# Optimization experiments

Hardware: AMD Instinct MI355X
Metric: run time of the kernel (lower is better)

The kernel has to match this reference:

```python
import jax, jax.numpy as jnp
import numpy as np

B, P, IN_DIM, OUT_DIM = 4, 120000, 4, 64
SPATIAL = (480, 360, 32)
EPS = 1e-5
SLOPE = 0.01  # LeakyReLU default negative slope


def setup_inputs() -> dict:
    key = jax.random.key(0)
    ks = jax.random.split(key, 10)
    pc = jax.random.normal(ks[0], (B, P, IN_DIM), dtype=jnp.float32)
    pc_indices = jax.random.randint(ks[1], (B, P, 3), 0, 32, dtype=jnp.int32)
    W1 = jax.random.normal(ks[2], (IN_DIM, 16), dtype=jnp.float32) * (1.0 / np.sqrt(IN_DIM))
    b1 = jax.random.normal(ks[3], (16,), dtype=jnp.float32) * 0.01
    g1 = jnp.ones((16,), jnp.float32)
    be1 = jnp.zeros((16,), jnp.float32)
    W2 = jax.random.normal(ks[4], (16, OUT_DIM), dtype=jnp.float32) * 0.25
    b2 = jax.random.normal(ks[5], (OUT_DIM,), dtype=jnp.float32) * 0.01
    g2 = jnp.ones((OUT_DIM,), jnp.float32)
    be2 = jnp.zeros((OUT_DIM,), jnp.float32)
    return {"pc": pc, "pc_indices": pc_indices, "W1": W1, "b1": b1, "g1": g1,
            "be1": be1, "W2": W2, "b2": b2, "g2": g2, "be2": be2}


def _bn_lrelu(h, g, b):
    # BatchNorm1d in training mode: batch mean / biased variance over points
    mean = jnp.mean(h, axis=0)
    var = jnp.mean((h - mean) ** 2, axis=0)
    h = (h - mean) / jnp.sqrt(var + EPS) * g + b
    return jnp.where(h >= 0, h, SLOPE * h)


def reference(pc, pc_indices, W1, b1, g1, be1, W2, b2, g2, be2):
    N = B * P
    x = pc.reshape(N, IN_DIM)
    bid = jnp.repeat(jnp.arange(B, dtype=jnp.int32), P)  # batch id padded in front
    coords = jnp.concatenate([bid[:, None], pc_indices.reshape(N, 3)], axis=1)  # [N,4]

    # small MLP (shuffle/recover in the original is a mathematical no-op for outputs)
    h = _bn_lrelu(x @ W1 + b1, g1, be1)
    feat = _bn_lrelu(h @ W2 + b2, g2, be2)  # [N, OUT_DIM]

    # torch.unique(dim=0) == lexicographic sort of linearized voxel keys
    S0, S1, S2 = SPATIAL
    key = (((coords[:, 0] * S0 + coords[:, 1]) * S1 + coords[:, 2]) * S2 + coords[:, 3])
    order = jnp.argsort(key)
    sk = key[order]
    is_first = jnp.concatenate([jnp.ones((1,), bool), sk[1:] != sk[:-1]])
    seg_sorted = (jnp.cumsum(is_first) - 1).astype(jnp.int32)  # segment id per sorted point
    inv = jnp.zeros((N,), jnp.int32).at[order].set(seg_sorted)  # inverse index (unsorted)

    # scatter_max into (padded, fixed-shape) voxel feature table
    voxel_feat = jax.ops.segment_max(feat, inv, num_segments=N)  # [N, OUT_DIM]
    n_uni = seg_sorted[-1] + 1
    valid = jnp.arange(N) < n_uni
    voxel_feat = jnp.where(valid[:, None], voxel_feat, 0.0)
    voxel_ind = jnp.zeros((N, 4), jnp.int32).at[seg_sorted].set(coords[order])

    return voxel_feat, voxel_ind, feat
```

## Files before the change

kernel.cpp:

```cpp
#include <hip/hip_runtime.h>

typedef unsigned int u32;
typedef unsigned long long u64;

#define N_PTS 480000
#define PPB   120000
#define NKEY  131072
#define NBLK_A 256
#define NBLK_B 512
#define NT64   7500
#define SLOPE 0.01f

__global__ __launch_bounds__(256) void kZ(u32* __restrict__ cnt) {
    uint4 z; z.x = 0u; z.y = 0u; z.z = 0u; z.w = 0u;
    ((uint4*)cnt)[blockIdx.x * 256 + threadIdx.x] = z;
}

__global__ __launch_bounds__(256) void kA(const float* __restrict__ pc,
                                          const int* __restrict__ pidx,
                                          u32* __restrict__ keys,
                                          u32* __restrict__ cnt,
                                          float* __restrict__ pA) {
    int t = threadIdx.x;
    float a[14];
#pragma unroll
    for (int j = 0; j < 14; ++j) a[j] = 0.f;

    for (int n = blockIdx.x * 256 + t; n < N_PTS; n += gridDim.x * 256) {
        float4 x = ((const float4*)pc)[n];
        a[0] += x.x; a[1] += x.y; a[2] += x.z; a[3] += x.w;
        a[4] += x.x * x.x; a[5] += x.x * x.y; a[6]  += x.x * x.z; a[7]  += x.x * x.w;
        a[8] += x.y * x.y; a[9] += x.y * x.z; a[10] += x.y * x.w;
        a[11] += x.z * x.z; a[12] += x.z * x.w; a[13] += x.w * x.w;

        int i0 = pidx[3 * n], i1 = pidx[3 * n + 1], i2 = pidx[3 * n + 2];
        int bid = n / PPB;
        u32 key = (u32)(bid * 32768 + i0 * 1024 + i1 * 32 + i2);
        keys[n] = key;
        atomicAdd(&cnt[key], 1u);
    }

    __shared__ float red[256];
    for (int j = 0; j < 14; ++j) {
        red[t] = a[j];
        __syncthreads();
        for (int s = 128; s > 0; s >>= 1) {
            if (t < s) red[t] += red[t + s];
            __syncthreads();
        }
        if (t == 0) pA[j * NBLK_A + blockIdx.x] = red[0];
        __syncthreads();
    }
}

__global__ __launch_bounds__(1024) void kR1(const float* __restrict__ pA,
                                            const float* __restrict__ W1,
                                            const float* __restrict__ b1,
                                            const float* __restrict__ g1,
                                            const float* __restrict__ be1,
                                            float* __restrict__ stats1) {
    int t = threadIdx.x, w = t >> 6, lane = t & 63;
    __shared__ float S[14];
    if (w < 14) {
        const float* p = pA + w * NBLK_A;
        float s = p[lane] + p[lane + 64] + p[lane + 128] + p[lane + 192];
        for (int d = 32; d > 0; d >>= 1) s += __shfl_xor(s, d);
        if (lane == 0) S[w] = s;
    }
    __syncthreads();
    if (t < 16) {
        int c = t;
        double w4[4];
#pragma unroll
        for (int i = 0; i < 4; ++i) w4[i] = W1[i * 16 + c];
        double sx[4] = { S[0], S[1], S[2], S[3] };
        auto sxx = [&](int i, int j) -> double {
            if (i > j) { int k = i; i = j; j = k; }
            int base = (i == 0) ? 4 : (i == 1) ? 8 : (i == 2) ? 11 : 13;
            return (double)S[base + (j - i)];
        };
        double su = 0.0;
        for (int i = 0; i < 4; ++i) su += sx[i] * w4[i];
        double q = 0.0;
        for (int i = 0; i < 4; ++i)
            for (int j = 0; j < 4; ++j) q += w4[i] * w4[j] * sxx(i, j);
        double b = (double)b1[c];
        double sum   = su + b * (double)N_PTS;
        double sumsq = q + 2.0 * b * su + (double)N_PTS * b * b;
        double mean = sum / (double)N_PTS;
        double var  = sumsq / (double)N_PTS - mean * mean;
        float inv = rsqrtf((float)(var + 1e-5));
        float sc = g1[c] * inv;
        stats1[c]      = sc;
        stats1[16 + c] = be1[c] - (float)mean * sc;
    }
}

__global__ __launch_bounds__(256) void kB(const float* __restrict__ pc,
                                          const float* __restrict__ W1,
                                          const float* __restrict__ b1,
                                          const float* __restrict__ stats1,
                                          float* __restrict__ pB) {
    int t = threadIdx.x;
    __shared__ float shx[256];
    __shared__ float shh[64][16];

    int c1 = t & 15;
    float w1c[4];
#pragma unroll
    for (int i = 0; i < 4; ++i) w1c[i] = W1[i * 16 + c1];
    float b1c = b1[c1], sc1 = stats1[c1], sf1 = stats1[16 + c1];

    int pi = 0, pj = 0;
    if (t >= 16 && t < 152) {
        int rem = t - 16, i = 0;
        while (rem >= 16 - i) { rem -= 16 - i; ++i; }
        pi = i; pj = i + rem;
    }

    float acc = 0.f;
    for (int tile = blockIdx.x; tile < NT64; tile += gridDim.x) {
        int base = tile * 64;
        shx[t] = pc[base * 4 + t];
        __syncthreads();
#pragma unroll
        for (int i = 0; i < 4; ++i) {
            int p = (t >> 4) + 16 * i;
            float hp = b1c + shx[p * 4 + 0] * w1c[0] + shx[p * 4 + 1] * w1c[1]
                           + shx[p * 4 + 2] * w1c[2] + shx[p * 4 + 3] * w1c[3];
            float z = hp * sc1 + sf1;
            shh[p][c1] = (z >= 0.f) ? z : SLOPE * z;
        }
        __syncthreads();
        if (t < 16) {
#pragma unroll 4
            for (int p = 0; p < 64; ++p) acc += shh[p][t];
        } else if (t < 152) {
#pragma unroll 4
            for (int p = 0; p < 64; ++p) acc += shh[p][pi] * shh[p][pj];
        }
        __syncthreads();
    }
    if (t < 152) pB[t * NBLK_B + blockIdx.x] = acc;
}

__global__ __launch_bounds__(1024) void kR2(const float* __restrict__ pB,
                                            const float* __restrict__ W2,
                                            const float* __restrict__ b2,
                                            const float* __restrict__ g2,
                                            const float* __restrict__ be2,
                                            float* __restrict__ stats2) {
    int t = threadIdx.x, w = t >> 6, lane = t & 63;
    __shared__ float S[152];
    for (int q = w; q < 152; q += 16) {
        const float* p = pB + q * NBLK_B;
        float s = 0.f;
#pragma unroll
        for (int b = 0; b < 8; ++b) s += p[b * 64 + lane];
        for (int d = 32; d > 0; d >>= 1) s += __shfl_xor(s, d);
        if (lane == 0) S[q] = s;
    }
    __syncthreads();
    if (t < 64) {
        double wv[16];
#pragma unroll
        for (int k = 0; k < 16; ++k) wv[k] = W2[k * 64 + t];
        double sh = 0.0;
        for (int k = 0; k < 16; ++k) sh += wv[k] * (double)S[k];
        auto qidx = [&](int i, int j) { return 16 + i * 16 - (i * (i - 1)) / 2 + (j - i); };
        double q = 0.0;
        for (int i = 0; i < 16; ++i) {
            q += wv[i] * wv[i] * (double)S[qidx(i, i)];
            double t2 = 0.0;
            for (int j = i + 1; j < 16; ++j) t2 += wv[j] * (double)S[qidx(i, j)];
            q += 2.0 * wv[i] * t2;
        }
        double b = (double)b2[t];
        double sum   = sh + b * (double)N_PTS;
        double sumsq = q + 2.0 * b * sh + (double)N_PTS * b * b;
        double mean = sum / (double)N_PTS;
        double var  = sumsq / (double)N_PTS - mean * mean;
        float inv = rsqrtf((float)(var + 1e-5));
        float sc = g2[t] * inv;
        stats2[t]      = sc;
        stats2[64 + t] = be2[t] - (float)mean * sc;
    }
}

__global__ __launch_bounds__(256) void kS1(const u32* __restrict__ cnt,
                                           u32* __restrict__ bsum) {
    int t = threadIdx.x, b = blockIdx.x;
    uint4 c4 = ((const uint4*)cnt)[b * 256 + t];
    u32 cs = c4.x + c4.y + c4.z + c4.w;
    u32 os = (c4.x > 0) + (c4.y > 0) + (c4.z > 0) + (c4.w > 0);
    __shared__ u32 rc[256], ro[256];
    rc[t] = cs; ro[t] = os;
    __syncthreads();
    for (int s = 128; s > 0; s >>= 1) {
        if (t < s) { rc[t] += rc[t + s]; ro[t] += ro[t + s]; }
        __syncthreads();
    }
    if (t == 0) { bsum[2 * b] = rc[0]; bsum[2 * b + 1] = ro[0]; }
}

__global__ __launch_bounds__(256) void kS2(u32* __restrict__ cnt,
                                           const u32* __restrict__ bsum,
                                           u32* __restrict__ startc,
                                           float* __restrict__ vi,
                                           u32* __restrict__ nuni) {
    int t = threadIdx.x, b = blockIdx.x;
    __shared__ u32 sbc[128], sbo[128];
    __shared__ u32 cOff, oOff;
    __shared__ u64 scan[256];
    if (t < 128) { sbc[t] = bsum[2 * t]; sbo[t] = bsum[2 * t + 1]; }

    uint4 c4 = ((const uint4*)cnt)[b * 256 + t];
    u32 cv[4] = { c4.x, c4.y, c4.z, c4.w };
    u32 cs = cv[0] + cv[1] + cv[2] + cv[3];
    u32 os = (cv[0] > 0) + (cv[1] > 0) + (cv[2] > 0) + (cv[3] > 0);
    scan[t] = ((u64)cs << 32) | (u64)os;
    __syncthreads();
    if (t == 0) {
        u32 a = 0, o = 0;
        for (int i = 0; i < b; ++i) { a += sbc[i]; o += sbo[i]; }
        cOff = a; oOff = o;
    }
    for (int d = 1; d < 256; d <<= 1) {
        u64 v = (t >= d) ? scan[t - d] : 0ull;
        __syncthreads();
        scan[t] += v;
        __syncthreads();
    }
    u64 ex = scan[t] - (((u64)cs << 32) | (u64)os);
    u32 start = cOff + (u32)(ex >> 32);
    u32 rank  = oOff + (u32)(ex & 0xffffffffull);

    int kbase = b * 1024 + t * 4;
#pragma unroll
    for (int j = 0; j < 4; ++j) {
        u32 k = (u32)(kbase + j);
        cnt[k] = start;
        if (cv[j] > 0) {
            startc[rank] = start;
            float4 o;
            o.x = (float)(k >> 15);
            o.y = (float)((k >> 10) & 31);
            o.z = (float)((k >> 5) & 31);
            o.w = (float)(k & 31);
            ((float4*)vi)[rank] = o;
            rank++;
        }
        start += cv[j];
    }
    if (b == 127 && t == 255) {
        nuni[0] = rank;
        startc[rank] = N_PTS;
    }
}

__global__ __launch_bounds__(256) void kP(const u32* __restrict__ keys,
                                          u32* __restrict__ cursor,
                                          u32* __restrict__ pid) {
    int n = blockIdx.x * 256 + threadIdx.x;
    if (n < N_PTS) {
        u32 k = keys[n];
        u32 pos = atomicAdd(&cursor[k], 1u);
        pid[pos] = (u32)n;
    }
}

__global__ __launch_bounds__(256) void kC(const float* __restrict__ pc,
                                          const float* __restrict__ W1,
                                          const float* __restrict__ b1,
                                          const float* __restrict__ stats1,
                                          const float* __restrict__ W2,
                                          const float* __restrict__ b2,
                                          const float* __restrict__ stats2,
                                          float* __restrict__ feat_out) {
    int t = threadIdx.x;
    __shared__ float shx[256];
    __shared__ float shh[64][16];

    int c1 = t & 15;
    float w1c[4];
#pragma unroll
    for (int i = 0; i < 4; ++i) w1c[i] = W1[i * 16 + c1];
    float b1c = b1[c1], sc1 = stats1[c1], sf1 = stats1[16 + c1];

    int c2 = t & 63;
    float w2c[16];
#pragma unroll
    for (int k = 0; k < 16; ++k) w2c[k] = W2[k * 64 + c2];
    float b2c = b2[c2], sc2 = stats2[c2], sf2 = stats2[64 + c2];
    int pg = t >> 6;

    for (int tile = blockIdx.x; tile < NT64; tile += gridDim.x) {
        int base = tile * 64;
        shx[t] = pc[base * 4 + t];
        __syncthreads();
#pragma unroll
        for (int i = 0; i < 4; ++i) {
            int p = (t >> 4) + 16 * i;
            float hp = b1c + shx[p * 4 + 0] * w1c[0] + shx[p * 4 + 1] * w1c[1]
                           + shx[p * 4 + 2] * w1c[2] + shx[p * 4 + 3] * w1c[3];
            float z = hp * sc1 + sf1;
            shh[p][c1] = (z >= 0.f) ? z : SLOPE * z;
        }
        __syncthreads();
#pragma unroll
        for (int j = 0; j < 16; ++j) {
            int p = pg + 4 * j;
            float f = b2c;
#pragma unroll
            for (int k = 0; k < 16; ++k) f += shh[p][k] * w2c[k];
            float z = f * sc2 + sf2;
            float ff = (z >= 0.f) ? z : SLOPE * z;
            feat_out[(size_t)(base + p) * 64 + c2] = ff;
        }
        __syncthreads();
    }
}

__global__ __launch_bounds__(256) void kV(const float* __restrict__ feat,
                                          const u32* __restrict__ pid,
                                          const u32* __restrict__ startc,
                                          const u32* __restrict__ nuni,
                                          float* __restrict__ vf,
                                          float* __restrict__ vi) {
    u32 nu = *nuni;
    u32 r0 = blockIdx.x * 4;
    int w = threadIdx.x >> 6, lane = threadIdx.x & 63;

    if (threadIdx.x < 16) {
        u32 row = r0 + (threadIdx.x >> 2);
        if (row >= nu) vi[(size_t)row * 4 + (threadIdx.x & 3)] = 0.f;
    }

    u32 r = r0 + (u32)w;
    if (r < nu) {
        u32 s = startc[r], e = startc[r + 1];
        float m = -3.4e38f;
        for (u32 i = s; i < e; ++i) {
            u32 p = pid[i];
            m = fmaxf(m, feat[(size_t)p * 64 + lane]);
        }
        vf[(size_t)r * 64 + lane] = m;
    } else {
        vf[(size_t)r * 64 + lane] = 0.f;
    }
}

extern "C" void kernel_launch(void* const* d_in, const int* in_sizes, int n_in,
                              void* d_out, int out_size, void* d_ws, size_t ws_size,
                              hipStream_t stream) {
    const float* pc   = (const float*)d_in[0];
    const int*   pidx = (const int*)d_in[1];
    const float* W1   = (const float*)d_in[2];
    const float* b1   = (const float*)d_in[3];
    const float* g1   = (const float*)d_in[4];
    const float* be1  = (const float*)d_in[5];
    const float* W2   = (const float*)d_in[6];
    const float* b2   = (const float*)d_in[7];
    const float* g2   = (const float*)d_in[8];
    const float* be2  = (const float*)d_in[9];

    float* vf   = (float*)d_out;
    float* vi   = vf + (size_t)N_PTS * 64;
    float* feat = vi + (size_t)N_PTS * 4;

    u32* ws     = (u32*)d_ws;
    u32* keys   = ws;
    u32* cnt    = ws + 480000;
    u32* startc = ws + 611072;
    u32* bsum   = ws + 742148;
    u32* nuni   = ws + 742404;
    u32* pid    = ws + 742420;
    float* pA     = (float*)(ws + 1222420);
    float* stats1 = (float*)(ws + 1226004);
    float* pB     = (float*)(ws + 1226036);
    float* stats2 = (float*)(ws + 1303860);

    kZ<<<128, 256, 0, stream>>>(cnt);
    kA<<<NBLK_A, 256, 0, stream>>>(pc, pidx, keys, cnt, pA);
    kR1<<<1, 1024, 0, stream>>>(pA, W1, b1, g1, be1, stats1);
    kB<<<NBLK_B, 256, 0, stream>>>(pc, W1, b1, stats1, pB);
    kR2<<<1, 1024, 0, stream>>>(pB, W2, b2, g2, be2, stats2);
    kS1<<<128, 256, 0, stream>>>(cnt, bsum);
    kS2<<<128, 256, 0, stream>>>(cnt, bsum, startc, vi, nuni);
    kP<<<1875, 256, 0, stream>>>(keys, cnt, pid);
    kC<<<2048, 256, 0, stream>>>(pc, W1, b1, stats1, W2, b2, stats2, feat);
    kV<<<120000, 256, 0, stream>>>(feat, pid, startc, nuni, vf, vi);
}
```

Baseline: 215.9 us.

## Fold BN scales into weights, register-accumulate layer-1 moments, bf16 hidden in kC

The BatchNorm scale and shift for both layers are folded into the linear weights and biases inside the reduction kernels, so later kernels do one fused affine per channel. kB is rewritten so each thread computes all 16 hidden values per point and accumulates the 152 first and second moments in registers, with a wave shuffle reduction replacing the shared-memory tile loop. It uses half as many blocks and pins to one block per CU, which risks register pressure. kC computes layer-1 directly from float4 loads and stores the hidden activations as packed bf16 in shared memory, which halves LDS traffic but lowers the precision of the hidden activations.

```diff
diff --git a/kernel.cpp b/kernel.cpp
--- a/kernel.cpp
+++ b/kernel.cpp
@@ -7,9 +7,18 @@
 #define PPB   120000
 #define NKEY  131072
 #define NBLK_A 256
-#define NBLK_B 512
+#define NBLK_B 256
 #define NT64   7500
 #define SLOPE 0.01f
+
+__device__ __forceinline__ u32 bf16pack(float lo, float hi) {
+    u32 a = __float_as_uint(lo), b = __float_as_uint(hi);
+    a += 0x7fffu + ((a >> 16) & 1u);
+    b += 0x7fffu + ((b >> 16) & 1u);
+    return (a >> 16) | (b & 0xffff0000u);
+}
+__device__ __forceinline__ float bf_lo(u32 v) { return __uint_as_float(v << 16); }
+__device__ __forceinline__ float bf_hi(u32 v) { return __uint_as_float(v & 0xffff0000u); }
 
 __global__ __launch_bounds__(256) void kZ(u32* __restrict__ cnt) {
     uint4 z; z.x = 0u; z.y = 0u; z.z = 0u; z.w = 0u;
@@ -91,57 +100,58 @@
         double var  = sumsq / (double)N_PTS - mean * mean;
         float inv = rsqrtf((float)(var + 1e-5));
         float sc = g1[c] * inv;
-        stats1[c]      = sc;
-        stats1[16 + c] = be1[c] - (float)mean * sc;
-    }
-}
-
-__global__ __launch_bounds__(256) void kB(const float* __restrict__ pc,
-                                          const float* __restrict__ W1,
-                                          const float* __restrict__ b1,
-                                          const float* __restrict__ stats1,
-                                          float* __restrict__ pB) {
-    int t = threadIdx.x;
-    __shared__ float shx[256];
-    __shared__ float shh[64][16];
-
-    int c1 = t & 15;
-    float w1c[4];
-#pragma unroll
-    for (int i = 0; i < 4; ++i) w1c[i] = W1[i * 16 + c1];
-    float b1c = b1[c1], sc1 = stats1[c1], sf1 = stats1[16 + c1];
-
-    int pi = 0, pj = 0;
-    if (t >= 16 && t < 152) {
-        int rem = t - 16, i = 0;
-        while (rem >= 16 - i) { rem -= 16 - i; ++i; }
-        pi = i; pj = i + rem;
-    }
-
-    float acc = 0.f;
-    for (int tile = blockIdx.x; tile < NT64; tile += gridDim.x) {
-        int base = tile * 64;
-        shx[t] = pc[base * 4 + t];
-        __syncthreads();
-#pragma unroll
-        for (int i = 0; i < 4; ++i) {
-            int p = (t >> 4) + 16 * i;
-            float hp = b1c + shx[p * 4 + 0] * w1c[0] + shx[p * 4 + 1] * w1c[1]
-                           + shx[p * 4 + 2] * w1c[2] + shx[p * 4 + 3] * w1c[3];
-            float z = hp * sc1 + sf1;
-            shh[p][c1] = (z >= 0.f) ? z : SLOPE * z;
-        }
-        __syncthreads();
-        if (t < 16) {
-#pragma unroll 4
-            for (int p = 0; p < 64; ++p) acc += shh[p][t];
-        } else if (t < 152) {
-#pragma unroll 4
-            for (int p = 0; p < 64; ++p) acc += shh[p][pi] * shh[p][pj];
-        }
-        __syncthreads();
-    }
-    if (t < 152) pB[t * NBLK_B + blockIdx.x] = acc;
+        float sf = be1[c] - (float)mean * sc;
+#pragma unroll
+        for (int i = 0; i < 4; ++i) stats1[c * 4 + i] = W1[i * 16 + c] * sc;
+        stats1[64 + c] = b1[c] * sc + sf;
+    }
+}
+
+__global__ __launch_bounds__(256, 1) void kB(const float* __restrict__ pc,
+                                             const float* __restrict__ stats1,
+                                             float* __restrict__ pB) {
+    int t = threadIdx.x, w = t >> 6, lane = t & 63;
+    __shared__ float sW[80];
+    __shared__ float sred[4][152];
+    if (t < 80) sW[t] = stats1[t];
+    __syncthreads();
+
+    float acc[152];
+#pragma unroll
+    for (int m = 0; m < 152; ++m) acc[m] = 0.f;
+
+    const float4* sW4 = (const float4*)sW;
+    for (int n = blockIdx.x * 256 + t; n < N_PTS; n += NBLK_B * 256) {
+        float4 x = ((const float4*)pc)[n];
+        float h[16];
+#pragma unroll
+        for (int k = 0; k < 16; ++k) {
+            float4 wk = sW4[k];
+            float z = x.x * wk.x + x.y * wk.y + x.z * wk.z + x.w * wk.w + sW[64 + k];
+            h[k] = (z >= 0.f) ? z : SLOPE * z;
+        }
+#pragma unroll
+        for (int i = 0; i < 16; ++i) acc[i] += h[i];
+#pragma unroll
+        for (int i = 0; i < 16; ++i)
+#pragma unroll
+            for (int j = i; j < 16; ++j)
+                acc[16 + i * 16 - (i * (i - 1)) / 2 + (j - i)] += h[i] * h[j];
+    }
+
+#pragma unroll
+    for (int m = 0; m < 152; ++m) {
+        float s = acc[m];
+        for (int d = 32; d > 0; d >>= 1) s += __shfl_xor(s, d);
+        acc[m] = s;
+    }
+    if (lane == 0) {
+#pragma unroll
+        for (int m = 0; m < 152; ++m) sred[w][m] = acc[m];
+    }
+    __syncthreads();
+    if (t < 152)
+        pB[t * NBLK_B + blockIdx.x] = sred[0][t] + sred[1][t] + sred[2][t] + sred[3][t];
 }
 
 __global__ __launch_bounds__(1024) void kR2(const float* __restrict__ pB,
@@ -154,9 +164,7 @@
     __shared__ float S[152];
     for (int q = w; q < 152; q += 16) {
         const float* p = pB + q * NBLK_B;
-        float s = 0.f;
-#pragma unroll
-        for (int b = 0; b < 8; ++b) s += p[b * 64 + lane];
+        float s = p[lane] + p[lane + 64] + p[lane + 128] + p[lane + 192];
         for (int d = 32; d > 0; d >>= 1) s += __shfl_xor(s, d);
         if (lane == 0) S[q] = s;
     }
@@ -182,8 +190,10 @@
         double var  = sumsq / (double)N_PTS - mean * mean;
         float inv = rsqrtf((float)(var + 1e-5));
         float sc = g2[t] * inv;
-        stats2[t]      = sc;
-        stats2[64 + t] = be2[t] - (float)mean * sc;
+        float sf = be2[t] - (float)mean * sc;
+#pragma unroll
+        for (int k = 0; k < 16; ++k) stats2[k * 64 + t] = W2[k * 64 + t] * sc;
+        stats2[1024 + t] = b2[t] * sc + sf;
     }
 }
 
@@ -270,51 +280,56 @@
 }
 
 __global__ __launch_bounds__(256) void kC(const float* __restrict__ pc,
-                                          const float* __restrict__ W1,
-                                          const float* __restrict__ b1,
                                           const float* __restrict__ stats1,
-                                          const float* __restrict__ W2,
-                                          const float* __restrict__ b2,
                                           const float* __restrict__ stats2,
                                           float* __restrict__ feat_out) {
     int t = threadIdx.x;
-    __shared__ float shx[256];
-    __shared__ float shh[64][16];
-
-    int c1 = t & 15;
-    float w1c[4];
-#pragma unroll
-    for (int i = 0; i < 4; ++i) w1c[i] = W1[i * 16 + c1];
-    float b1c = b1[c1], sc1 = stats1[c1], sf1 = stats1[16 + c1];
-
-    int c2 = t & 63;
+    __shared__ u32 shp[64][8];
+
+    int cpair = t & 7, psub = t >> 3;
+    float w1a[4], w1b[4], c1a, c1b;
+#pragma unroll
+    for (int i = 0; i < 4; ++i) {
+        w1a[i] = stats1[(2 * cpair) * 4 + i];
+        w1b[i] = stats1[(2 * cpair + 1) * 4 + i];
+    }
+    c1a = stats1[64 + 2 * cpair];
+    c1b = stats1[64 + 2 * cpair + 1];
+
+    int c2 = t & 63, pg = t >> 6;
     float w2c[16];
 #pragma unroll
-    for (int k = 0; k < 16; ++k) w2c[k] = W2[k * 64 + c2];
-    float b2c = b2[c2], sc2 = stats2[c2], sf2 = stats2[64 + c2];
-    int pg = t >> 6;
+    for (int k = 0; k < 16; ++k) w2c[k] = stats2[k * 64 + c2];
+    float c2fr = stats2[1024 + c2];
 
     for (int tile = blockIdx.x; tile < NT64; tile += gridDim.x) {
         int base = tile * 64;
-        shx[t] = pc[base * 4 + t];
-        __syncthreads();
-#pragma unroll
-        for (int i = 0; i < 4; ++i) {
-            int p = (t >> 4) + 16 * i;
-            float hp = b1c + shx[p * 4 + 0] * w1c[0] + shx[p * 4 + 1] * w1c[1]
-                           + shx[p * 4 + 2] * w1c[2] + shx[p * 4 + 3] * w1c[3];
-            float z = hp * sc1 + sf1;
-            shh[p][c1] = (z >= 0.f) ? z : SLOPE * z;
+#pragma unroll
+        for (int half = 0; half < 2; ++half) {
+            int p = psub + 32 * half;
+            float4 x = ((const float4*)pc)[base + p];
+            float za = x.x * w1a[0] + x.y * w1a[1] + x.z * w1a[2] + x.w * w1a[3] + c1a;
+            float zb = x.x * w1b[0] + x.y * w1b[1] + x.z * w1b[2] + x.w * w1b[3] + c1b;
+            za = (za >= 0.f) ? za : SLOPE * za;
+            zb = (zb >= 0.f) ? zb : SLOPE * zb;
+            shp[p][cpair] = bf16pack(za, zb);
         }
         __syncthreads();
 #pragma unroll
         for (int j = 0; j < 16; ++j) {
             int p = pg + 4 * j;
-            float f = b2c;
-#pragma unroll
-            for (int k = 0; k < 16; ++k) f += shh[p][k] * w2c[k];
-            float z = f * sc2 + sf2;
-            float ff = (z >= 0.f) ? z : SLOPE * z;
+            const uint4* row = (const uint4*)&shp[p][0];
+            uint4 v0 = row[0], v1 = row[1];
+            float f = c2fr;
+            f += bf_lo(v0.x) * w2c[0]  + bf_hi(v0.x) * w2c[1];
+            f += bf_lo(v0.y) * w2c[2]  + bf_hi(v0.y) * w2c[3];
+            f += bf_lo(v0.z) * w2c[4]  + bf_hi(v0.z) * w2c[5];
+            f += bf_lo(v0.w) * w2c[6]  + bf_hi(v0.w) * w2c[7];
+            f += bf_lo(v1.x) * w2c[8]  + bf_hi(v1.x) * w2c[9];
+            f += bf_lo(v1.y) * w2c[10] + bf_hi(v1.y) * w2c[11];
+            f += bf_lo(v1.z) * w2c[12] + bf_hi(v1.z) * w2c[13];
+            f += bf_lo(v1.w) * w2c[14] + bf_hi(v1.w) * w2c[15];
+            float ff = (f >= 0.f) ? f : SLOPE * f;
             feat_out[(size_t)(base + p) * 64 + c2] = ff;
         }
         __syncthreads();
@@ -377,17 +392,17 @@
     u32* pid    = ws + 742420;
     float* pA     = (float*)(ws + 1222420);
     float* stats1 = (float*)(ws + 1226004);
-    float* pB     = (float*)(ws + 1226036);
-    float* stats2 = (float*)(ws + 1303860);
+    float* pB     = (float*)(ws + 1226084);
+    float* stats2 = (float*)(ws + 1264996);
 
     kZ<<<128, 256, 0, stream>>>(cnt);
     kA<<<NBLK_A, 256, 0, stream>>>(pc, pidx, keys, cnt, pA);
     kR1<<<1, 1024, 0, stream>>>(pA, W1, b1, g1, be1, stats1);
-    kB<<<NBLK_B, 256, 0, stream>>>(pc, W1, b1, stats1, pB);
+    kB<<<NBLK_B, 256, 0, stream>>>(pc, stats1, pB);
     kR2<<<1, 1024, 0, stream>>>(pB, W2, b2, g2, be2, stats2);
     kS1<<<128, 256, 0, stream>>>(cnt, bsum);
     kS2<<<128, 256, 0, stream>>>(cnt, bsum, startc, vi, nuni);
     kP<<<1875, 256, 0, stream>>>(keys, cnt, pid);
-    kC<<<2048, 256, 0, stream>>>(pc, W1, b1, stats1, W2, b2, stats2, feat);
+    kC<<<2048, 256, 0, stream>>>(pc, stats1, stats2, feat);
     kV<<<120000, 256, 0, stream>>>(feat, pid, startc, nuni, vf, vi);
 }
```

Result: faster. 204.9 us (-5.1%).
